# Optimization experiments

Measured on AMD Instinct MI355X. Metric: run time of the kernel, lower is better.

Reference implementation:

```python
import jax, jax.numpy as jnp
import numpy as np

B, D, H, O, E, K = 16384, 128, 512, 128, 8, 2
T = 1.0
EPS = float(np.finfo(float).eps)  # combine() zero-fill epsilon


def cv_squared(v):
    # torch .var() is unbiased (ddof=1)
    return jnp.var(v, ddof=1) / (jnp.mean(v) ** 2 + 1e-10)


def setup_inputs() -> dict:
    key = jax.random.key(0)
    k0, k1, k2, k3, k4, k5 = jax.random.split(key, 6)
    x = jax.random.normal(k0, (B, D), dtype=jnp.float32)
    w_gate = jax.random.normal(k1, (D, E), dtype=jnp.float32) * 0.02
    w1 = jax.random.normal(k2, (E, D, H), dtype=jnp.float32) * (1.0 / np.sqrt(D))
    b1 = jax.random.normal(k3, (E, H), dtype=jnp.float32) * 0.01
    w2 = jax.random.normal(k4, (E, H, O), dtype=jnp.float32) * (1.0 / np.sqrt(H))
    b2 = jax.random.normal(k5, (E, O), dtype=jnp.float32) * 0.01
    return {"x": x, "w_gate": w_gate, "w1": w1, "b1": b1, "w2": w2, "b2": b2}


def reference(x, w_gate, w1, b1, w2, b2):
    # ---- noisy top-k gating (eval mode: clean logits, no noise) ----
    logits = x @ w_gate                                   # [B, E]
    top_logits, top_idx = jax.lax.top_k(logits, K)        # [B, K]
    top_gates = jax.nn.softmax(top_logits / T, axis=-1)   # [B, K]
    gates = jnp.zeros_like(logits).at[jnp.arange(x.shape[0])[:, None], top_idx].set(top_gates)

    importance = gates.sum(0)                              # [E]
    load = (gates > 0).sum(0).astype(jnp.float32)          # [E]
    loss = cv_squared(importance) + cv_squared(load)

    # ---- experts (dense gate-weighted form of dispatch/combine) ----
    # output[b] = Sum_i gates[b,i] * expert_i(x[b]); zero gates contribute nothing,
    # identical math to SparseDispatcher's gather / per-expert MLP / scatter-add.
    h = jax.nn.relu(jnp.einsum('bd,edh->beh', x, w1) + b1[None])   # [B, E, H]
    y_e = jnp.einsum('beh,eho->beo', h, w2) + b2[None]             # [B, E, O]
    y = jnp.einsum('be,beo->bo', gates, y_e)                       # [B, O]
    # combine(): combined[combined == 0] = eps
    y = jnp.where(y == 0, jnp.asarray(EPS, y.dtype), y)
    return y, loss
```

## Files before the change

### kernel.cpp

```cpp
#include <hip/hip_runtime.h>
#include <hip/hip_bf16.h>
#include <math.h>

#define NB 16384
#define ND 128
#define NH 512
#define NO 128
#define NE 8
#define NCH 16
#define EPSF 2.2204460492503131e-16f

using bf16x8 = __attribute__((ext_vector_type(8))) short;
using f32x16 = __attribute__((ext_vector_type(16))) float;
using uint2v = __attribute__((ext_vector_type(2))) unsigned;

#define WS_BLKCNT 0u
#define WS_BLKIMP 8192u
#define WS_TOKID  16384u
#define WS_TOKGG  1064960u
#define WS_XBF    1196032u
#define WS_W1F    5390336u
#define WS_W2F    6438912u
#define WS_YSTAGE 7487488u

__device__ __forceinline__ unsigned f2bf(float f){
  unsigned u = __float_as_uint(f);
  u += 0x7FFFu + ((u >> 16) & 1u);
  return u >> 16;
}
__device__ __forceinline__ unsigned cvtpk(float lo, float hi){
  unsigned r;
  asm("v_cvt_pk_bf16_f32 %0, %1, %2" : "=v"(r) : "v"(lo), "v"(hi));
  return r;
}
__device__ __forceinline__ void gld16(const void* g, void* l){
  __builtin_amdgcn_global_load_lds((const __attribute__((address_space(1))) void*)g,
                                   (__attribute__((address_space(3))) void*)l, 16, 0, 0);
}

__global__ __launch_bounds__(256) void prep_kernel(
    const float* __restrict__ x, const float* __restrict__ wg,
    const float* __restrict__ w1, const float* __restrict__ w2,
    unsigned short* __restrict__ xbf, unsigned short* __restrict__ w1f,
    unsigned short* __restrict__ w2f, int* __restrict__ blk_cnt,
    float* __restrict__ blk_imp, int* __restrict__ tok_ids, float2* __restrict__ tok_gg){
  int bx = blockIdx.x, tid = threadIdx.x;
  if (bx >= 512){
    int u = (bx - 512)*256 + tid;
    int o = u & 127, hb = (u>>7)&3, c = (u>>9)&15, e = u>>13;
    int h0 = c*32 + (hb>>1)*16 + (hb&1)*8;
    const float* src = w2 + (size_t)e*NH*NO + (size_t)h0*NO + o;
    unsigned q[4];
    #pragma unroll
    for (int p = 0; p < 4; ++p)
      q[p] = f2bf(src[(2*p)*NO]) | (f2bf(src[(2*p+1)*NO]) << 16);
    *(uint4*)(w2f + (size_t)u*8) = make_uint4(q[0], q[1], q[2], q[3]);
    return;
  }
  if (bx >= 256){
    int u = (bx - 256)*256 + tid;
    int h32 = u & 31, db = (u>>5)&15, c = (u>>9)&15, e = u>>13;
    int d0 = (db>>1)*16 + (db&1)*8;
    int hg = c*32 + h32;
    const float* src = w1 + (size_t)e*ND*NH + (size_t)d0*NH + hg;
    unsigned q[4];
    #pragma unroll
    for (int p = 0; p < 4; ++p)
      q[p] = f2bf(src[(2*p)*NH]) | (f2bf(src[(2*p+1)*NH]) << 16);
    *(uint4*)(w1f + (size_t)u*8) = make_uint4(q[0], q[1], q[2], q[3]);
    return;
  }
  __shared__ int   lcnt[NE];
  __shared__ float limp[NE];
  if (tid < NE){ lcnt[tid] = 0; limp[tid] = 0.f; }
  __syncthreads();
  int tok  = bx*64 + (tid >> 2);
  int part = tid & 3;
  const float4* xr4 = (const float4*)(x + (size_t)tok*ND);
  double acc[NE];
  #pragma unroll
  for (int e = 0; e < NE; ++e) acc[e] = 0.0;
  #pragma unroll
  for (int j = 0; j < 8; ++j){
    int f4 = part + j*4;
    float4 v = xr4[f4];
    uint2 p;
    p.x = f2bf(v.x) | (f2bf(v.y) << 16);
    p.y = f2bf(v.z) | (f2bf(v.w) << 16);
    *(uint2*)(xbf + (size_t)tok*ND + f4*4) = p;
    const float4* wr = (const float4*)(wg + f4*32);
    float vm[4] = {v.x, v.y, v.z, v.w};
    #pragma unroll
    for (int m = 0; m < 4; ++m){
      float4 wa = wr[2*m], wb = wr[2*m+1];
      double d = (double)vm[m];
      acc[0] += d*(double)wa.x; acc[1] += d*(double)wa.y;
      acc[2] += d*(double)wa.z; acc[3] += d*(double)wa.w;
      acc[4] += d*(double)wb.x; acc[5] += d*(double)wb.y;
      acc[6] += d*(double)wb.z; acc[7] += d*(double)wb.w;
    }
  }
  #pragma unroll
  for (int e = 0; e < NE; ++e){
    acc[e] += __shfl_xor(acc[e], 1);
    acc[e] += __shfl_xor(acc[e], 2);
  }
  if (part == 0){
    int i0 = 0;
    double l0 = acc[0];
    #pragma unroll
    for (int e = 1; e < NE; ++e) if (acc[e] > l0){ l0 = acc[e]; i0 = e; }
    int i1 = (i0 == 0) ? 1 : 0;
    double l1 = acc[i1];
    #pragma unroll
    for (int e = 0; e < NE; ++e) if (e != i0 && acc[e] > l1){ l1 = acc[e]; i1 = e; }
    float e1 = expf((float)(l1 - l0));
    float g0 = 1.0f/(1.0f + e1);
    float g1 = e1/(1.0f + e1);
    int s0 = atomicAdd(&lcnt[i0], 1);
    int s1 = atomicAdd(&lcnt[i1], 1);
    atomicAdd(&limp[i0], g0);
    atomicAdd(&limp[i1], g1);
    tok_gg[tok] = make_float2(g0, g1);
    tok_ids[i0*32768 + bx*128 + s0] = tok;
    tok_ids[i1*32768 + bx*128 + s1] = tok | (1 << 30);
  }
  __syncthreads();
  if (tid < NE){
    blk_cnt[bx*8 + tid] = lcnt[tid];
    blk_imp[bx*8 + tid] = limp[tid];
  }
}

__global__ __launch_bounds__(256) void expert_kernel(
    const unsigned short* __restrict__ xbf, const unsigned short* __restrict__ w1f,
    const unsigned short* __restrict__ w2f, const float* __restrict__ b1,
    const float* __restrict__ b2, const int* __restrict__ blk_cnt,
    const int* __restrict__ tok_ids, const float2* __restrict__ tok_gg,
    unsigned short* __restrict__ ystage){
  __shared__ char L[44032];
  int* cnt_l  = (int*)(L + 32768);
  int* gp     = (int*)(L + 40960);
  int* totl   = (int*)(L + 41984);
  int* tbase  = (int*)(L + 42016);
  int* sl_tok = (int*)(L + 42056);
  int tid = threadIdx.x;
  {
    int4 a = *(const int4*)(blk_cnt + tid*8);
    int4 c = *(const int4*)(blk_cnt + tid*8 + 4);
    cnt_l[0*256+tid]=a.x; cnt_l[1*256+tid]=a.y; cnt_l[2*256+tid]=a.z; cnt_l[3*256+tid]=a.w;
    cnt_l[4*256+tid]=c.x; cnt_l[5*256+tid]=c.y; cnt_l[6*256+tid]=c.z; cnt_l[7*256+tid]=c.w;
  }
  __syncthreads();
  {
    int e8 = tid >> 5, g8 = tid & 31;
    int s8 = 0;
    #pragma unroll
    for (int i = 0; i < 8; ++i) s8 += cnt_l[e8*256 + g8*8 + i];
    gp[tid] = s8;
    __syncthreads();
    #pragma unroll
    for (int st = 1; st < 32; st <<= 1){
      int add = (g8 >= st) ? gp[tid - st] : 0;
      __syncthreads();
      gp[tid] += add;
      __syncthreads();
    }
    if (g8 == 31) totl[e8] = gp[tid];
    __syncthreads();
    if (tid == 0){
      tbase[0] = 0;
      #pragma unroll
      for (int e = 0; e < NE; ++e) tbase[e+1] = tbase[e] + ((totl[e] + 127) >> 7);
    }
    __syncthreads();
  }
  int b = blockIdx.x;
  if (b >= tbase[8]) return;
  int e = 0;
  #pragma unroll
  for (int ee = 1; ee < NE; ++ee) if (tbase[ee] <= b) e = ee;
  int n_e  = totl[e];
  int base = (b - tbase[e])*128;
  if (tid < 128){
    int s = base + tid;
    if (s >= n_e) s = n_e - 1;
    int g = 0;
    #pragma unroll
    for (int st = 16; st; st >>= 1){
      int c = g + st;
      if (c <= 31 && gp[e*32 + c - 1] <= s) g = c;
    }
    int acc2 = g ? gp[e*32 + g - 1] : 0;
    int gb = g*8;
    while (true){
      int c2 = cnt_l[e*256 + gb];
      if (acc2 + c2 > s) break;
      acc2 += c2; ++gb;
    }
    sl_tok[tid] = tok_ids[e*32768 + gb*128 + (s - acc2)];
  }
  __syncthreads();

  int wid = tid >> 6, lane = tid & 63, l31 = lane & 31, hi = lane >> 5;
  char* w1buf = L;
  char* w2buf = L + 16384;
  const char* g1base = (const char*)w1f + (size_t)e*131072;
  const char* g2base = (const char*)w2f + (size_t)e*131072;

  int raw0 = sl_tok[wid*32 + l31];
  int tok0 = raw0 & 0x3FFFFFFF;
  bf16x8 xfrag[8];
  #pragma unroll
  for (int k = 0; k < 8; ++k)
    xfrag[k] = *(const bf16x8*)(xbf + (size_t)tok0*ND + (k*2 + hi)*8);

#define STAGE(c, bsel) do { \
    const char* _g1 = g1base + (size_t)(c)*8192 + wid*1024 + lane*16; \
    const char* _g2 = g2base + (size_t)(c)*8192 + wid*1024 + lane*16; \
    char* _l1 = w1buf + (bsel)*8192 + wid*1024; \
    char* _l2 = w2buf + (bsel)*8192 + wid*1024; \
    _Pragma("unroll") \
    for (int _s = 0; _s < 2; ++_s){ \
      gld16(_g1 + _s*4096, _l1 + _s*4096); \
      gld16(_g2 + _s*4096, _l2 + _s*4096); \
    } \
  } while(0)

  STAGE(0, 0);
  f32x16 yacc[4];
  #pragma unroll
  for (int ot = 0; ot < 4; ++ot)
    #pragma unroll
    for (int i = 0; i < 16; ++i) yacc[ot][i] = 0.f;
  __syncthreads();

  for (int c = 0; c < NCH; ++c){
    int bb = c & 1;
    if (c + 1 < NCH) STAGE(c + 1, bb ^ 1);
    f32x16 hacc;
    #pragma unroll
    for (int i = 0; i < 16; ++i) hacc[i] = 0.f;
    #pragma unroll
    for (int k = 0; k < 8; ++k){
      bf16x8 a = *(const bf16x8*)(w1buf + bb*8192 + (k*2 + hi)*512 + l31*16);
      hacc = __builtin_amdgcn_mfma_f32_32x32x16_bf16(a, xfrag[k], hacc, 0, 0, 0);
    }
    const float4* b1p = (const float4*)(b1 + e*NH + c*32 + hi*4);
    float dv[16];
    #pragma unroll
    for (int g = 0; g < 4; ++g){
      float4 bv = b1p[2*g];
      dv[4*g+0] = fmaxf(hacc[4*g+0] + bv.x, 0.f);
      dv[4*g+1] = fmaxf(hacc[4*g+1] + bv.y, 0.f);
      dv[4*g+2] = fmaxf(hacc[4*g+2] + bv.z, 0.f);
      dv[4*g+3] = fmaxf(hacc[4*g+3] + bv.w, 0.f);
    }
    unsigned A0 = cvtpk(dv[0], dv[1]),   A1 = cvtpk(dv[2], dv[3]);
    unsigned A2 = cvtpk(dv[4], dv[5]),   A3 = cvtpk(dv[6], dv[7]);
    unsigned A4 = cvtpk(dv[8], dv[9]),   A5 = cvtpk(dv[10], dv[11]);
    unsigned A6 = cvtpk(dv[12], dv[13]), A7 = cvtpk(dv[14], dv[15]);
    uint2v r0 = __builtin_amdgcn_permlane32_swap(A0, A2, false, false);
    uint2v r1 = __builtin_amdgcn_permlane32_swap(A1, A3, false, false);
    uint2v r2 = __builtin_amdgcn_permlane32_swap(A4, A6, false, false);
    uint2v r3 = __builtin_amdgcn_permlane32_swap(A5, A7, false, false);
    union { unsigned u[4]; bf16x8 v; } fa, fb;
    fa.u[0] = r0[0]; fa.u[1] = r1[0]; fa.u[2] = r0[1]; fa.u[3] = r1[1];
    fb.u[0] = r2[0]; fb.u[1] = r3[0]; fb.u[2] = r2[1]; fb.u[3] = r3[1];
    bf16x8 aht0 = fa.v, aht1 = fb.v;
    #pragma unroll
    for (int ot = 0; ot < 4; ++ot){
      bf16x8 bf0 = *(const bf16x8*)(w2buf + bb*8192 + hi*2048 + (ot*32 + l31)*16);
      yacc[ot] = __builtin_amdgcn_mfma_f32_32x32x16_bf16(aht0, bf0, yacc[ot], 0, 0, 0);
      bf16x8 bf1 = *(const bf16x8*)(w2buf + bb*8192 + (2 + hi)*2048 + (ot*32 + l31)*16);
      yacc[ot] = __builtin_amdgcn_mfma_f32_32x32x16_bf16(aht1, bf1, yacc[ot], 0, 0, 0);
    }
    __syncthreads();
  }
#undef STAGE
  float b2v[4];
  #pragma unroll
  for (int ot = 0; ot < 4; ++ot) b2v[ot] = b2[e*NO + ot*32 + l31];
  #pragma unroll
  for (int r = 0; r < 16; ++r){
    int row = (r & 3) + 8*(r >> 2) + 4*hi;
    int slot = base + wid*32 + row;
    if (slot < n_e){
      int rw = sl_tok[wid*32 + row];
      int tk = rw & 0x3FFFFFFF, wh = (rw >> 30) & 1;
      float2 gg = tok_gg[tk];
      float g = wh ? gg.y : gg.x;
      unsigned short* dst = ystage + ((size_t)tk*2 + wh)*NO + l31;
      #pragma unroll
      for (int ot = 0; ot < 4; ++ot)
        dst[ot*32] = (unsigned short)f2bf((yacc[ot][r] + b2v[ot]) * g);
    }
  }
}

__global__ __launch_bounds__(256) void combine_kernel(
    const unsigned short* __restrict__ ystage, const int* __restrict__ blk_cnt,
    const float* __restrict__ blk_imp, float* __restrict__ y){
  if (blockIdx.x == 0){
    __shared__ int   scnt[32];
    __shared__ float simp[32];
    int tid = threadIdx.x, lane = tid & 63, wid = tid >> 6;
    int4 ca = *(const int4*)(blk_cnt + tid*8);
    int4 cb = *(const int4*)(blk_cnt + tid*8 + 4);
    float4 ia = *(const float4*)(blk_imp + tid*8);
    float4 ib = *(const float4*)(blk_imp + tid*8 + 4);
    int   cv[8] = {ca.x, ca.y, ca.z, ca.w, cb.x, cb.y, cb.z, cb.w};
    float iv[8] = {ia.x, ia.y, ia.z, ia.w, ib.x, ib.y, ib.z, ib.w};
    #pragma unroll
    for (int e = 0; e < NE; ++e){
      int   rc = cv[e];
      float ri = iv[e];
      #pragma unroll
      for (int st = 1; st < 64; st <<= 1){
        rc += __shfl_xor(rc, st);
        ri += __shfl_xor(ri, st);
      }
      if (lane == 0){ scnt[e*4 + wid] = rc; simp[e*4 + wid] = ri; }
    }
    __syncthreads();
    if (tid == 0){
      double si = 0, sqi = 0, sl = 0, sql = 0;
      #pragma unroll
      for (int e = 0; e < NE; ++e){
        double a = (double)(simp[e*4] + simp[e*4+1] + simp[e*4+2] + simp[e*4+3]);
        double bb = (double)(scnt[e*4] + scnt[e*4+1] + scnt[e*4+2] + scnt[e*4+3]);
        si += a; sqi += a*a; sl += bb; sql += bb*bb;
      }
      double mi = si/8.0, vi = (sqi - 8.0*mi*mi)/7.0;
      double ml = sl/8.0, vl = (sql - 8.0*ml*ml)/7.0;
      y[NB*NO] = (float)(vi/(mi*mi + 1e-10) + vl/(ml*ml + 1e-10));
    }
  }
  int idx = blockIdx.x*256 + threadIdx.x;
  int tk = idx >> 4, q = idx & 15;
  const unsigned short* r0 = ystage + (size_t)tk*256 + q*8;
  uint4 a = *(const uint4*)r0;
  uint4 bq = *(const uint4*)(r0 + 128);
  unsigned aw[4] = {a.x, a.y, a.z, a.w};
  unsigned bw[4] = {bq.x, bq.y, bq.z, bq.w};
  float outs[8];
  #pragma unroll
  for (int i = 0; i < 4; ++i){
    float vlo = __uint_as_float(aw[i] << 16)         + __uint_as_float(bw[i] << 16);
    float vhi = __uint_as_float(aw[i] & 0xFFFF0000u) + __uint_as_float(bw[i] & 0xFFFF0000u);
    outs[2*i]   = (vlo == 0.f) ? EPSF : vlo;
    outs[2*i+1] = (vhi == 0.f) ? EPSF : vhi;
  }
  float4 o0 = {outs[0], outs[1], outs[2], outs[3]};
  float4 o1 = {outs[4], outs[5], outs[6], outs[7]};
  float* dst = y + (size_t)tk*128 + q*8;
  *(float4*)dst     = o0;
  *(float4*)(dst+4) = o1;
}

extern "C" void kernel_launch(void* const* d_in, const int* in_sizes, int n_in,
                              void* d_out, int out_size, void* d_ws, size_t ws_size,
                              hipStream_t stream){
  (void)in_sizes; (void)n_in; (void)out_size; (void)ws_size;
  const float* x  = (const float*)d_in[0];
  const float* wg = (const float*)d_in[1];
  const float* w1 = (const float*)d_in[2];
  const float* b1 = (const float*)d_in[3];
  const float* w2 = (const float*)d_in[4];
  const float* b2 = (const float*)d_in[5];
  float* out = (float*)d_out;
  char* ws = (char*)d_ws;
  int*            blk_cnt = (int*)(ws + WS_BLKCNT);
  float*          blk_imp = (float*)(ws + WS_BLKIMP);
  int*            tok_ids = (int*)(ws + WS_TOKID);
  float2*         tok_gg  = (float2*)(ws + WS_TOKGG);
  unsigned short* xbf     = (unsigned short*)(ws + WS_XBF);
  unsigned short* w1f     = (unsigned short*)(ws + WS_W1F);
  unsigned short* w2f     = (unsigned short*)(ws + WS_W2F);
  unsigned short* ystage  = (unsigned short*)(ws + WS_YSTAGE);

  prep_kernel<<<768, 256, 0, stream>>>(x, wg, w1, w2, xbf, w1f, w2f,
                                       blk_cnt, blk_imp, tok_ids, tok_gg);
  expert_kernel<<<264, 256, 0, stream>>>(xbf, w1f, w2f, b1, b2,
                                         blk_cnt, tok_ids, tok_gg, ystage);
  combine_kernel<<<1024, 256, 0, stream>>>(ystage, blk_cnt, blk_imp, out);
}
```

Measured before the change: 48.39 us.

## Deepen expert-kernel weight staging to 64-column chunks with manual waitcnt pipelining

The expert kernel now stages W1/W2 in 64-column phases (32KB per slot, double-buffered into 64KB of LDS) instead of 32-column chunks. Each phase uses explicit vmcnt waits and raw s_barrier in place of __syncthreads so the next phase's loads stay in flight, and raises wave priority around the MFMA runs. b1 is staged into LDS once. The per-expert prefix scan now uses wave shuffles instead of an LDS scan with repeated barriers. The larger LDS footprint may reduce how many blocks fit per CU.

```diff
diff --git a/kernel.cpp b/kernel.cpp
--- a/kernel.cpp
+++ b/kernel.cpp
@@ -7,7 +7,6 @@
 #define NH 512
 #define NO 128
 #define NE 8
-#define NCH 16
 #define EPSF 2.2204460492503131e-16f
 
 using bf16x8 = __attribute__((ext_vector_type(8))) short;
@@ -138,18 +137,20 @@
     const float* __restrict__ b2, const int* __restrict__ blk_cnt,
     const int* __restrict__ tok_ids, const float2* __restrict__ tok_gg,
     unsigned short* __restrict__ ystage){
-  __shared__ char L[44032];
-  int* cnt_l  = (int*)(L + 32768);
-  int* gp     = (int*)(L + 40960);
-  int* totl   = (int*)(L + 41984);
-  int* tbase  = (int*)(L + 42016);
-  int* sl_tok = (int*)(L + 42056);
+  __shared__ char L[77440];
+  char*  wbuf   = L;
+  int*   cnt_l  = (int*)(L + 65536);
+  int*   gp     = (int*)(L + 73728);
+  int*   sl_tok = (int*)(L + 74752);
+  float* b1s    = (float*)(L + 75264);
+  int*   totl   = (int*)(L + 77312);
+  int*   tbase  = (int*)(L + 77344);
   int tid = threadIdx.x;
   {
     int4 a = *(const int4*)(blk_cnt + tid*8);
-    int4 c = *(const int4*)(blk_cnt + tid*8 + 4);
-    cnt_l[0*256+tid]=a.x; cnt_l[1*256+tid]=a.y; cnt_l[2*256+tid]=a.z; cnt_l[3*256+tid]=a.w;
-    cnt_l[4*256+tid]=c.x; cnt_l[5*256+tid]=c.y; cnt_l[6*256+tid]=c.z; cnt_l[7*256+tid]=c.w;
+    int4 c4 = *(const int4*)(blk_cnt + tid*8 + 4);
+    cnt_l[0*256+tid]=a.x;  cnt_l[1*256+tid]=a.y;  cnt_l[2*256+tid]=a.z;  cnt_l[3*256+tid]=a.w;
+    cnt_l[4*256+tid]=c4.x; cnt_l[5*256+tid]=c4.y; cnt_l[6*256+tid]=c4.z; cnt_l[7*256+tid]=c4.w;
   }
   __syncthreads();
   {
@@ -157,24 +158,22 @@
     int s8 = 0;
     #pragma unroll
     for (int i = 0; i < 8; ++i) s8 += cnt_l[e8*256 + g8*8 + i];
-    gp[tid] = s8;
-    __syncthreads();
+    int pre = s8;
     #pragma unroll
     for (int st = 1; st < 32; st <<= 1){
-      int add = (g8 >= st) ? gp[tid - st] : 0;
-      __syncthreads();
-      gp[tid] += add;
-      __syncthreads();
-    }
-    if (g8 == 31) totl[e8] = gp[tid];
-    __syncthreads();
-    if (tid == 0){
-      tbase[0] = 0;
-      #pragma unroll
-      for (int e = 0; e < NE; ++e) tbase[e+1] = tbase[e] + ((totl[e] + 127) >> 7);
-    }
-    __syncthreads();
-  }
+      int o = __shfl_up(pre, st, 32);
+      if (g8 >= st) pre += o;
+    }
+    gp[tid] = pre;
+    if (g8 == 31) totl[e8] = pre;
+  }
+  __syncthreads();
+  if (tid == 0){
+    tbase[0] = 0;
+    #pragma unroll
+    for (int e = 0; e < NE; ++e) tbase[e+1] = tbase[e] + ((totl[e] + 127) >> 7);
+  }
+  __syncthreads();
   int b = blockIdx.x;
   if (b >= tbase[8]) return;
   int e = 0;
@@ -203,8 +202,6 @@
   __syncthreads();
 
   int wid = tid >> 6, lane = tid & 63, l31 = lane & 31, hi = lane >> 5;
-  char* w1buf = L;
-  char* w2buf = L + 16384;
   const char* g1base = (const char*)w1f + (size_t)e*131072;
   const char* g2base = (const char*)w2f + (size_t)e*131072;
 
@@ -214,14 +211,18 @@
   #pragma unroll
   for (int k = 0; k < 8; ++k)
     xfrag[k] = *(const bf16x8*)(xbf + (size_t)tok0*ND + (k*2 + hi)*8);
-
-#define STAGE(c, bsel) do { \
-    const char* _g1 = g1base + (size_t)(c)*8192 + wid*1024 + lane*16; \
-    const char* _g2 = g2base + (size_t)(c)*8192 + wid*1024 + lane*16; \
-    char* _l1 = w1buf + (bsel)*8192 + wid*1024; \
-    char* _l2 = w2buf + (bsel)*8192 + wid*1024; \
+  asm volatile("s_waitcnt vmcnt(0)" ::: "memory");
+  __builtin_amdgcn_sched_barrier(0);
+  if (wid < 2)
+    gld16((const char*)(b1 + e*NH) + wid*1024 + lane*16, (char*)b1s + wid*1024);
+
+#define STAGE(p, slot) do { \
+    const char* _g1 = g1base + (size_t)(p)*16384 + wid*1024 + lane*16; \
+    const char* _g2 = g2base + (size_t)(p)*16384 + wid*1024 + lane*16; \
+    char* _l1 = wbuf + (slot)*32768 + wid*1024; \
+    char* _l2 = wbuf + (slot)*32768 + 16384 + wid*1024; \
     _Pragma("unroll") \
-    for (int _s = 0; _s < 2; ++_s){ \
+    for (int _s = 0; _s < 4; ++_s){ \
       gld16(_g1 + _s*4096, _l1 + _s*4096); \
       gld16(_g2 + _s*4096, _l2 + _s*4096); \
     } \
@@ -233,51 +234,67 @@
   for (int ot = 0; ot < 4; ++ot)
     #pragma unroll
     for (int i = 0; i < 16; ++i) yacc[ot][i] = 0.f;
-  __syncthreads();
-
-  for (int c = 0; c < NCH; ++c){
-    int bb = c & 1;
-    if (c + 1 < NCH) STAGE(c + 1, bb ^ 1);
-    f32x16 hacc;
-    #pragma unroll
-    for (int i = 0; i < 16; ++i) hacc[i] = 0.f;
-    #pragma unroll
-    for (int k = 0; k < 8; ++k){
-      bf16x8 a = *(const bf16x8*)(w1buf + bb*8192 + (k*2 + hi)*512 + l31*16);
-      hacc = __builtin_amdgcn_mfma_f32_32x32x16_bf16(a, xfrag[k], hacc, 0, 0, 0);
-    }
-    const float4* b1p = (const float4*)(b1 + e*NH + c*32 + hi*4);
-    float dv[16];
-    #pragma unroll
-    for (int g = 0; g < 4; ++g){
-      float4 bv = b1p[2*g];
-      dv[4*g+0] = fmaxf(hacc[4*g+0] + bv.x, 0.f);
-      dv[4*g+1] = fmaxf(hacc[4*g+1] + bv.y, 0.f);
-      dv[4*g+2] = fmaxf(hacc[4*g+2] + bv.z, 0.f);
-      dv[4*g+3] = fmaxf(hacc[4*g+3] + bv.w, 0.f);
-    }
-    unsigned A0 = cvtpk(dv[0], dv[1]),   A1 = cvtpk(dv[2], dv[3]);
-    unsigned A2 = cvtpk(dv[4], dv[5]),   A3 = cvtpk(dv[6], dv[7]);
-    unsigned A4 = cvtpk(dv[8], dv[9]),   A5 = cvtpk(dv[10], dv[11]);
-    unsigned A6 = cvtpk(dv[12], dv[13]), A7 = cvtpk(dv[14], dv[15]);
-    uint2v r0 = __builtin_amdgcn_permlane32_swap(A0, A2, false, false);
-    uint2v r1 = __builtin_amdgcn_permlane32_swap(A1, A3, false, false);
-    uint2v r2 = __builtin_amdgcn_permlane32_swap(A4, A6, false, false);
-    uint2v r3 = __builtin_amdgcn_permlane32_swap(A5, A7, false, false);
-    union { unsigned u[4]; bf16x8 v; } fa, fb;
-    fa.u[0] = r0[0]; fa.u[1] = r1[0]; fa.u[2] = r0[1]; fa.u[3] = r1[1];
-    fb.u[0] = r2[0]; fb.u[1] = r3[0]; fb.u[2] = r2[1]; fb.u[3] = r3[1];
-    bf16x8 aht0 = fa.v, aht1 = fb.v;
-    #pragma unroll
-    for (int ot = 0; ot < 4; ++ot){
-      bf16x8 bf0 = *(const bf16x8*)(w2buf + bb*8192 + hi*2048 + (ot*32 + l31)*16);
-      yacc[ot] = __builtin_amdgcn_mfma_f32_32x32x16_bf16(aht0, bf0, yacc[ot], 0, 0, 0);
-      bf16x8 bf1 = *(const bf16x8*)(w2buf + bb*8192 + (2 + hi)*2048 + (ot*32 + l31)*16);
-      yacc[ot] = __builtin_amdgcn_mfma_f32_32x32x16_bf16(aht1, bf1, yacc[ot], 0, 0, 0);
-    }
-    __syncthreads();
+
+  #pragma unroll
+  for (int p = 0; p < 8; ++p){
+    int slot = p & 1;
+    if (p < 7) STAGE(p + 1, slot ^ 1);
+    if (p < 7) asm volatile("s_waitcnt vmcnt(8)" ::: "memory");
+    else       asm volatile("s_waitcnt vmcnt(0)" ::: "memory");
+    __builtin_amdgcn_sched_barrier(0);
+    __builtin_amdgcn_s_barrier();
+    const char* w1p = wbuf + slot*32768;
+    const char* w2p = wbuf + slot*32768 + 16384;
+    #pragma unroll
+    for (int sub = 0; sub < 2; ++sub){
+      int c32 = p*2 + sub;
+      f32x16 hacc;
+      #pragma unroll
+      for (int i = 0; i < 16; ++i) hacc[i] = 0.f;
+      __builtin_amdgcn_s_setprio(1);
+      #pragma unroll
+      for (int k = 0; k < 8; ++k){
+        bf16x8 a = *(const bf16x8*)(w1p + sub*8192 + (k*2 + hi)*512 + l31*16);
+        hacc = __builtin_amdgcn_mfma_f32_32x32x16_bf16(a, xfrag[k], hacc, 0, 0, 0);
+      }
+      __builtin_amdgcn_s_setprio(0);
+      float dv[16];
+      #pragma unroll
+      for (int g = 0; g < 4; ++g){
+        float4 bv = *(const float4*)(b1s + c32*32 + hi*4 + g*8);
+        dv[4*g+0] = fmaxf(hacc[4*g+0] + bv.x, 0.f);
+        dv[4*g+1] = fmaxf(hacc[4*g+1] + bv.y, 0.f);
+        dv[4*g+2] = fmaxf(hacc[4*g+2] + bv.z, 0.f);
+        dv[4*g+3] = fmaxf(hacc[4*g+3] + bv.w, 0.f);
+      }
+      unsigned A0 = cvtpk(dv[0], dv[1]),   A1 = cvtpk(dv[2], dv[3]);
+      unsigned A2 = cvtpk(dv[4], dv[5]),   A3 = cvtpk(dv[6], dv[7]);
+      unsigned A4 = cvtpk(dv[8], dv[9]),   A5 = cvtpk(dv[10], dv[11]);
+      unsigned A6 = cvtpk(dv[12], dv[13]), A7 = cvtpk(dv[14], dv[15]);
+      uint2v r0 = __builtin_amdgcn_permlane32_swap(A0, A2, false, false);
+      uint2v r1 = __builtin_amdgcn_permlane32_swap(A1, A3, false, false);
+      uint2v r2 = __builtin_amdgcn_permlane32_swap(A4, A6, false, false);
+      uint2v r3 = __builtin_amdgcn_permlane32_swap(A5, A7, false, false);
+      union { unsigned u[4]; bf16x8 v; } fa, fb;
+      fa.u[0] = r0[0]; fa.u[1] = r1[0]; fa.u[2] = r0[1]; fa.u[3] = r1[1];
+      fb.u[0] = r2[0]; fb.u[1] = r3[0]; fb.u[2] = r2[1]; fb.u[3] = r3[1];
+      bf16x8 aht0 = fa.v, aht1 = fb.v;
+      __builtin_amdgcn_s_setprio(1);
+      #pragma unroll
+      for (int ot = 0; ot < 4; ++ot){
+        bf16x8 bf0 = *(const bf16x8*)(w2p + sub*8192 + hi*2048 + (ot*32 + l31)*16);
+        yacc[ot] = __builtin_amdgcn_mfma_f32_32x32x16_bf16(aht0, bf0, yacc[ot], 0, 0, 0);
+        bf16x8 bf1 = *(const bf16x8*)(w2p + sub*8192 + (2 + hi)*2048 + (ot*32 + l31)*16);
+        yacc[ot] = __builtin_amdgcn_mfma_f32_32x32x16_bf16(aht1, bf1, yacc[ot], 0, 0, 0);
+      }
+      __builtin_amdgcn_s_setprio(0);
+    }
+    asm volatile("s_waitcnt lgkmcnt(0)" ::: "memory");
+    __builtin_amdgcn_sched_barrier(0);
+    __builtin_amdgcn_s_barrier();
   }
 #undef STAGE
+
   float b2v[4];
   #pragma unroll
   for (int ot = 0; ot < 4; ++ot) b2v[ot] = b2[e*NO + ot*32 + l31];
```

Result: no change. 47.65 us (-1.5%).
